# Optimization experiments

Hardware: AMD Instinct MI355X
Metric: run time of the kernel (lower is better)

Reference implementation:

```python
import jax, jax.numpy as jnp
import numpy as np

N_NODES = 100000


def setup_inputs() -> dict:
    key = jax.random.key(0)
    k1, k2, k3, k4, k5 = jax.random.split(key, 5)
    x = jax.random.normal(k1, (N_NODES, 256), dtype=jnp.float32)
    edge_index = jax.random.randint(k2, (2, 3200000), 0, N_NODES, dtype=jnp.int64)
    edge_weight = jax.random.uniform(k3, (3200000,), dtype=jnp.float32)
    W = jax.random.normal(k4, (256, 128), dtype=jnp.float32) / np.sqrt(256.0)
    b = jax.random.normal(k5, (128,), dtype=jnp.float32) * 0.01
    return {"x": x, "edge_index": edge_index, "edge_weight": edge_weight, "W": W, "b": b}


def reference(x, edge_index, edge_weight, W, b):
    # Dense linear projection: h = x @ W + b  -> [N, out_feats]
    h = x @ W + b
    # SpMM aggregation: out[dst] += w_e * h[src]
    src = edge_index[1]  # column indices (neighbors)
    dst = edge_index[0]  # row indices (output nodes)
    msgs = h[src] * edge_weight[:, None]  # [E, out_feats]
    out = jax.ops.segment_sum(msgs, dst, num_segments=x.shape[0])
    return out
```

## Files before the change

kernel.cpp:

```cpp
#include <hip/hip_runtime.h>

#define K_IN   256
#define N_OUT  128
#define BM     32
#define SCAN_CHUNK 1024
#define NBLK   512
#define BSHIFT 7
#define BNODES 128
#define CAP    8192
#define NKEY   2048
#define GEMM_BLOCKS 512

typedef short bf16x8 __attribute__((ext_vector_type(8)));
typedef float f32x4  __attribute__((ext_vector_type(4)));

static __device__ __forceinline__ unsigned short f2bf(float f) {
    unsigned u = __float_as_uint(f);
    unsigned r = (u + 0x7FFF + ((u >> 16) & 1)) >> 16;
    return (unsigned short)r;
}
static __device__ __forceinline__ float bf2f(unsigned short b) {
    return __uint_as_float(((unsigned)b) << 16);
}

__global__ __launch_bounds__(256) void hist_prep(
    const float* __restrict__ W, char* __restrict__ wbt,
    const int* __restrict__ ei, int* __restrict__ histG,
    int M, int E, int B, int chunk)
{
    __shared__ int bins[1024];
    const int tid = threadIdx.x;

    if (blockIdx.x >= NBLK) {
        const int t = (blockIdx.x - NBLK) * 256 + tid;
        if (t >= N_OUT * 32) return;
        const int n = t >> 5;
        const int c = t & 31;
        unsigned v[4];
#pragma unroll
        for (int p = 0; p < 4; ++p) {
            const unsigned lo = f2bf(W[(size_t)(c * 8 + 2 * p)     * N_OUT + n]);
            const unsigned hi = f2bf(W[(size_t)(c * 8 + 2 * p + 1) * N_OUT + n]);
            v[p] = lo | (hi << 16);
        }
        const int byte = n * 512 + ((c * 16) ^ ((n & 7) << 4));
        *reinterpret_cast<uint4*>(wbt + byte) = make_uint4(v[0], v[1], v[2], v[3]);
        return;
    }

    for (int i = tid; i < B; i += 256) bins[i] = 0;
    __syncthreads();
    const int beg = blockIdx.x * chunk;
    const int end = min(beg + chunk, E);
    for (int i = beg + tid; i < end; i += 256)
        atomicAdd(&bins[ei[i] >> BSHIFT], 1);
    __syncthreads();
    for (int i = tid; i < B; i += 256) histG[i * NBLK + blockIdx.x] = bins[i];
}

__global__ __launch_bounds__(256) void scan_block_sums(
    const int* __restrict__ cnt, int n, int* __restrict__ bsum)
{
    __shared__ int sd[256];
    const int base = blockIdx.x * SCAN_CHUNK + threadIdx.x * 4;
    int s = 0;
#pragma unroll
    for (int j = 0; j < 4; ++j) { const int idx = base + j; if (idx < n) s += cnt[idx]; }
    sd[threadIdx.x] = s; __syncthreads();
    for (int off = 128; off > 0; off >>= 1) {
        if (threadIdx.x < off) sd[threadIdx.x] += sd[threadIdx.x + off];
        __syncthreads();
    }
    if (threadIdx.x == 0) bsum[blockIdx.x] = sd[0];
}

__global__ __launch_bounds__(1024) void scan_sums(
    int* __restrict__ bsum, int nb, int* __restrict__ P, int n)
{
    __shared__ int sd[1024];
    const int t = threadIdx.x;
    const int v = (t < nb) ? bsum[t] : 0;
    sd[t] = v; __syncthreads();
    for (int off = 1; off < 1024; off <<= 1) {
        const int add = (t >= off) ? sd[t - off] : 0;
        __syncthreads();
        sd[t] += add;
        __syncthreads();
    }
    if (t < nb) bsum[t] = sd[t] - v;
    if (t == nb - 1) P[n] = sd[t];
}

__global__ __launch_bounds__(256) void scan_write_offsets(
    const int* __restrict__ cnt, int n, const int* __restrict__ bsum, int* __restrict__ P)
{
    __shared__ int sd[256];
    const int t = threadIdx.x;
    const int base = blockIdx.x * SCAN_CHUNK + t * 4;
    int v[4]; int s = 0;
#pragma unroll
    for (int j = 0; j < 4; ++j) { const int idx = base + j; v[j] = (idx < n) ? cnt[idx] : 0; s += v[j]; }
    sd[t] = s; __syncthreads();
    const int own = s;
    for (int off = 1; off < 256; off <<= 1) {
        const int add = (t >= off) ? sd[t - off] : 0;
        __syncthreads();
        sd[t] += add;
        __syncthreads();
    }
    int run = bsum[blockIdx.x] + (sd[t] - own);
#pragma unroll
    for (int j = 0; j < 4; ++j) {
        const int idx = base + j;
        if (idx < n) { P[idx] = run; run += v[j]; }
    }
}

__global__ __launch_bounds__(256) void gcn_gemm3(
    const float* __restrict__ x, const uint4* __restrict__ wbt,
    const float* __restrict__ bias, unsigned short* __restrict__ hb,
    int M, int ntiles)
{
    __shared__ uint4 smem4[81920 / 16];
    char* smem = (char*)smem4;
    const int tid = threadIdx.x;

    {
        uint4* wl = (uint4*)smem;
#pragma unroll
        for (int it = 0; it < 16; ++it) wl[it * 256 + tid] = wbt[it * 256 + tid];
    }

    const int lane = tid & 63;
    const int wv   = tid >> 6;
    const int wr   = wv >> 1;
    const int wc   = wv & 1;
    const int l15  = lane & 15;
    const int lk   = lane >> 4;

    const int  arow = wr * 16 + l15;
    const char* xrow = smem + 65536 + arow * 512;
    const int  aswz = (arow & 7) << 4;
    const int  bswz = (l15 & 7) << 4;
    const char* brow0 = smem + (size_t)(wc * 64 + l15) * 512;

    float bv[4];
#pragma unroll
    for (int j = 0; j < 4; ++j) bv[j] = bias[wc * 64 + j * 16 + l15];

    const int sr  = tid >> 3;
    const int sks = tid & 7;
    char* xbase   = smem + 65536 + sr * 512;
    const int swz = (sr & 7) << 4;

    for (int t = blockIdx.x; t < ntiles; t += gridDim.x) {
        const int row0 = t * BM;

        __syncthreads();
        {
            const int grow = row0 + sr;
            if (grow < M) {
                const float4* src = reinterpret_cast<const float4*>(x + (size_t)grow * K_IN + sks * 32);
#pragma unroll
                for (int q = 0; q < 8; ++q) {
                    const float4 f = src[q];
                    uint2 v;
                    v.x = (unsigned)f2bf(f.x) | ((unsigned)f2bf(f.y) << 16);
                    v.y = (unsigned)f2bf(f.z) | ((unsigned)f2bf(f.w) << 16);
                    const int kb = sks * 64 + q * 8;
                    *reinterpret_cast<uint2*>(xbase + (((kb & ~15) ^ swz) | (kb & 15))) = v;
                }
            } else {
                const uint2 z = make_uint2(0u, 0u);
#pragma unroll
                for (int q = 0; q < 8; ++q) {
                    const int kb = sks * 64 + q * 8;
                    *reinterpret_cast<uint2*>(xbase + (((kb & ~15) ^ swz) | (kb & 15))) = z;
                }
            }
        }
        __syncthreads();

        f32x4 acc[4] = {};
#pragma unroll
        for (int ks = 0; ks < 8; ++ks) {
            const int kb = ks * 64 + lk * 16;
            const bf16x8 a = *reinterpret_cast<const bf16x8*>(xrow + (kb ^ aswz));
            const int bk = kb ^ bswz;
#pragma unroll
            for (int j = 0; j < 4; ++j) {
                const bf16x8 b = *reinterpret_cast<const bf16x8*>(brow0 + j * (16 * 512) + bk);
                acc[j] = __builtin_amdgcn_mfma_f32_16x16x32_bf16(a, b, acc[j], 0, 0, 0);
            }
        }

#pragma unroll
        for (int j = 0; j < 4; ++j) {
            const int gcol = wc * 64 + j * 16 + l15;
#pragma unroll
            for (int r = 0; r < 4; ++r) {
                const int grow = row0 + wr * 16 + lk * 4 + r;
                if (grow < M)
                    hb[(size_t)grow * N_OUT + gcol] = f2bf(acc[j][r] + bv[j]);
            }
        }
    }
}

__global__ __launch_bounds__(256) void scatter_records(
    const int* __restrict__ ei, const float* __restrict__ ew, int E, int M, int B,
    const int* __restrict__ P, uint2* __restrict__ rec, int chunk)
{
    __shared__ int cur[1024];
    for (int i = threadIdx.x; i < B; i += 256) cur[i] = P[i * NBLK + blockIdx.x];
    __syncthreads();
    const int beg = blockIdx.x * chunk;
    const int end = min(beg + chunk, E);
    for (int i = beg + threadIdx.x; i < end; i += 256) {
        const int d = ei[i];
        const int s = ei[(size_t)E + i];
        const int pos = atomicAdd(&cur[d >> BSHIFT], 1);
        rec[pos] = make_uint2((unsigned)s | ((unsigned)(d & (BNODES - 1)) << 24),
                              __float_as_uint(ew[i]));
    }
}

__global__ __launch_bounds__(256) void sort_bucket(
    const int* __restrict__ P, uint2* __restrict__ rec,
    int* __restrict__ offsN, int* __restrict__ bflag, int M, int B)
{
    __shared__ uint2 srt[CAP];
    __shared__ int hist[NKEY];
    __shared__ int sd[256];

    const int b   = blockIdx.x;
    const int tid = threadIdx.x;
    const int beg = P[b * NBLK];
    const int end = P[(b + 1) * NBLK];
    const int cnt = end - beg;
    const int node0 = b << BSHIFT;

    for (int i = tid; i < NKEY; i += 256) hist[i] = 0;
    if (tid == 0) bflag[b] = (cnt <= CAP) ? 0 : 1;
    if (tid == 0 && b == B - 1) offsN[M] = end;
    __syncthreads();

    if (cnt > CAP) {
        if (tid < BNODES) {
            const int node = node0 + tid;
            if (node < M) offsN[node] = beg;
        }
        return;
    }

    for (int i = beg + tid; i < end; i += 256) {
        const uint2 r = rec[i];
        srt[i - beg] = r;
        const int key = ((r.x >> 24) << 4) | ((r.x & 0xFFFFFF) >> 13);
        atomicAdd(&hist[key], 1);
    }
    __syncthreads();

    const int base = tid * 8;
    int v[8]; int s = 0;
#pragma unroll
    for (int j = 0; j < 8; ++j) { v[j] = hist[base + j]; s += v[j]; }
    sd[tid] = s; __syncthreads();
    for (int off = 1; off < 256; off <<= 1) {
        const int add = (tid >= off) ? sd[tid - off] : 0;
        __syncthreads();
        sd[tid] += add;
        __syncthreads();
    }
    int run = sd[tid] - s;
#pragma unroll
    for (int j = 0; j < 8; ++j) { hist[base + j] = run; run += v[j]; }
    __syncthreads();

    if (tid < BNODES) {
        const int node = node0 + tid;
        if (node < M) offsN[node] = beg + hist[tid << 4];
    }
    __syncthreads();

    for (int i = tid; i < cnt; i += 256) {
        const uint2 r = srt[i];
        const int key = ((r.x >> 24) << 4) | ((r.x & 0xFFFFFF) >> 13);
        const int pos = atomicAdd(&hist[key], 1);
        rec[beg + pos] = r;
    }
}

__global__ __launch_bounds__(256) void gather_kernel(
    const int* __restrict__ offsN, const int* __restrict__ P,
    const int* __restrict__ bflag, const uint2* __restrict__ rec,
    const unsigned short* __restrict__ hb, float* __restrict__ out, int M)
{
    const int n = blockIdx.x * 4 + (threadIdx.x >> 6);
    if (n >= M) return;
    const int lane = threadIdx.x & 63;
    const int b = n >> BSHIFT;
    const unsigned* __restrict__ hb32 = reinterpret_cast<const unsigned*>(hb);

    float ax = 0.f, ay = 0.f;

    if (bflag[b] == 0) {
        const int beg = offsN[n], end = offsN[n + 1];
        int i = beg;
        for (; i + 16 <= end; i += 16) {
            unsigned u[16]; float w[16];
#pragma unroll
            for (int q = 0; q < 16; ++q) {
                const uint2 r = rec[i + q];
                w[q] = __uint_as_float(r.y);
                u[q] = hb32[(size_t)((r.x & 0xFFFFFF) << 6) + lane];
            }
#pragma unroll
            for (int q = 0; q < 16; ++q) {
                ax += w[q] * bf2f((unsigned short)u[q]);
                ay += w[q] * bf2f((unsigned short)(u[q] >> 16));
            }
        }
        for (; i + 8 <= end; i += 8) {
            unsigned u[8]; float w[8];
#pragma unroll
            for (int q = 0; q < 8; ++q) {
                const uint2 r = rec[i + q];
                w[q] = __uint_as_float(r.y);
                u[q] = hb32[(size_t)((r.x & 0xFFFFFF) << 6) + lane];
            }
#pragma unroll
            for (int q = 0; q < 8; ++q) {
                ax += w[q] * bf2f((unsigned short)u[q]);
                ay += w[q] * bf2f((unsigned short)(u[q] >> 16));
            }
        }
        for (; i < end; ++i) {
            const uint2 r = rec[i];
            const float w = __uint_as_float(r.y);
            const unsigned u = hb32[(size_t)((r.x & 0xFFFFFF) << 6) + lane];
            ax += w * bf2f((unsigned short)u);
            ay += w * bf2f((unsigned short)(u >> 16));
        }
    } else {
        const int beg = P[b * NBLK], end = P[(b + 1) * NBLK];
        const unsigned want = (unsigned)(n & (BNODES - 1));
        for (int i = beg; i < end; ++i) {
            const uint2 r = rec[i];
            if ((r.x >> 24) != want) continue;
            const float w = __uint_as_float(r.y);
            const unsigned u = hb32[(size_t)((r.x & 0xFFFFFF) << 6) + lane];
            ax += w * bf2f((unsigned short)u);
            ay += w * bf2f((unsigned short)(u >> 16));
        }
    }

    reinterpret_cast<float2*>(out + (size_t)n * N_OUT)[lane] = make_float2(ax, ay);
}

extern "C" void kernel_launch(void* const* d_in, const int* in_sizes, int n_in,
                              void* d_out, int out_size, void* d_ws, size_t ws_size,
                              hipStream_t stream)
{
    const float* x    = (const float*)d_in[0];
    const int*   ei   = (const int*)d_in[1];
    const float* ew   = (const float*)d_in[2];
    const float* W    = (const float*)d_in[3];
    const float* bias = (const float*)d_in[4];
    float* out = (float*)d_out;

    const int M = in_sizes[0] / K_IN;
    const int E = in_sizes[1] / 2;
    const int B = (M + BNODES - 1) >> BSHIFT;
    const int n = B * NBLK;
    const int nb = (n + SCAN_CHUNK - 1) / SCAN_CHUNK;
    const int chunk = (E + NBLK - 1) / NBLK;
    const int ntiles = (M + BM - 1) / BM;

    auto align256 = [](size_t v) { return (v + 255) & ~(size_t)255; };
    const size_t o_hb    = 0;
    const size_t o_hist  = align256(o_hb + (size_t)M * N_OUT * sizeof(unsigned short));
    const size_t o_P     = align256(o_hist + (size_t)n * sizeof(int));
    const size_t o_bsum  = align256(o_P + (size_t)(n + 1) * sizeof(int));
    const size_t o_offsN = align256(o_bsum + (size_t)1024 * sizeof(int));
    const size_t o_bflag = align256(o_offsN + (size_t)(M + 1) * sizeof(int));
    const size_t o_wbt   = align256(o_bflag + (size_t)B * sizeof(int));
    const size_t o_rec   = align256(o_wbt + (size_t)65536);

    unsigned short* hb    = (unsigned short*)((char*)d_ws + o_hb);
    int*            histG = (int*)((char*)d_ws + o_hist);
    int*            P     = (int*)((char*)d_ws + o_P);
    int*            bsum  = (int*)((char*)d_ws + o_bsum);
    int*            offsN = (int*)((char*)d_ws + o_offsN);
    int*            bflag = (int*)((char*)d_ws + o_bflag);
    char*           wbt   = (char*)d_ws + o_wbt;
    uint2*          rec   = (uint2*)((char*)d_ws + o_rec);

    hist_prep<<<NBLK + 16, 256, 0, stream>>>(W, wbt, ei, histG, M, E, B, chunk);
    gcn_gemm3<<<GEMM_BLOCKS, 256, 0, stream>>>(x, (const uint4*)wbt, bias, hb, M, ntiles);
    scan_block_sums<<<nb, 256, 0, stream>>>(histG, n, bsum);
    scan_sums<<<1, 1024, 0, stream>>>(bsum, nb, P, n);
    scan_write_offsets<<<nb, 256, 0, stream>>>(histG, n, bsum, P);
    scatter_records<<<NBLK, 256, 0, stream>>>(ei, ew, E, M, B, P, rec, chunk);
    sort_bucket<<<B, 256, 0, stream>>>(P, rec, offsN, bflag, M, B);
    gather_kernel<<<(M + 3) / 4, 256, 0, stream>>>(offsN, P, bflag, rec, hb, out, M);
}
```

Before: 240.6 us.

## Fuse GEMM and edge scatter into one kernel and swizzle gather blocks across XCDs

```diff
diff --git a/kernel.cpp b/kernel.cpp
--- a/kernel.cpp
+++ b/kernel.cpp
@@ -9,7 +9,7 @@
 #define BNODES 128
 #define CAP    8192
 #define NKEY   2048
-#define GEMM_BLOCKS 512
+#define NXCD   8
 
 typedef short bf16x8 __attribute__((ext_vector_type(8)));
 typedef float f32x4  __attribute__((ext_vector_type(4)));
@@ -116,14 +116,36 @@
     }
 }
 
-__global__ __launch_bounds__(256) void gcn_gemm3(
+__global__ __launch_bounds__(256) void gemm_scatter2(
     const float* __restrict__ x, const uint4* __restrict__ wbt,
     const float* __restrict__ bias, unsigned short* __restrict__ hb,
-    int M, int ntiles)
+    const int* __restrict__ ei, const float* __restrict__ ew,
+    const int* __restrict__ P, uint2* __restrict__ rec,
+    int M, int E, int B, int chunk, int ntiles)
 {
     __shared__ uint4 smem4[81920 / 16];
     char* smem = (char*)smem4;
     const int tid = threadIdx.x;
+
+    if (blockIdx.x & 1) {
+        int* cur = (int*)smem;
+        const int blk = blockIdx.x >> 1;
+        for (int i = tid; i < B; i += 256) cur[i] = P[i * NBLK + blk];
+        __syncthreads();
+        const int beg = blk * chunk;
+        const int end = min(beg + chunk, E);
+        for (int i = beg + tid; i < end; i += 256) {
+            const int d = ei[i];
+            const int s = ei[(size_t)E + i];
+            const int pos = atomicAdd(&cur[d >> BSHIFT], 1);
+            rec[pos] = make_uint2((unsigned)s | ((unsigned)(d & (BNODES - 1)) << 24),
+                                  __float_as_uint(ew[i]));
+        }
+        return;
+    }
+
+    const int gemm_id = blockIdx.x >> 1;
+    const int gstride = gridDim.x >> 1;
 
     {
         uint4* wl = (uint4*)smem;
@@ -153,7 +175,7 @@
     char* xbase   = smem + 65536 + sr * 512;
     const int swz = (sr & 7) << 4;
 
-    for (int t = blockIdx.x; t < ntiles; t += gridDim.x) {
+    for (int t = gemm_id; t < ntiles; t += gstride) {
         const int row0 = t * BM;
 
         __syncthreads();
@@ -207,24 +229,6 @@
     }
 }
 
-__global__ __launch_bounds__(256) void scatter_records(
-    const int* __restrict__ ei, const float* __restrict__ ew, int E, int M, int B,
-    const int* __restrict__ P, uint2* __restrict__ rec, int chunk)
-{
-    __shared__ int cur[1024];
-    for (int i = threadIdx.x; i < B; i += 256) cur[i] = P[i * NBLK + blockIdx.x];
-    __syncthreads();
-    const int beg = blockIdx.x * chunk;
-    const int end = min(beg + chunk, E);
-    for (int i = beg + threadIdx.x; i < end; i += 256) {
-        const int d = ei[i];
-        const int s = ei[(size_t)E + i];
-        const int pos = atomicAdd(&cur[d >> BSHIFT], 1);
-        rec[pos] = make_uint2((unsigned)s | ((unsigned)(d & (BNODES - 1)) << 24),
-                              __float_as_uint(ew[i]));
-    }
-}
-
 __global__ __launch_bounds__(256) void sort_bucket(
     const int* __restrict__ P, uint2* __restrict__ rec,
     int* __restrict__ offsN, int* __restrict__ bflag, int M, int B)
@@ -296,7 +300,14 @@
     const int* __restrict__ bflag, const uint2* __restrict__ rec,
     const unsigned short* __restrict__ hb, float* __restrict__ out, int M)
 {
-    const int n = blockIdx.x * 4 + (threadIdx.x >> 6);
+    const int nwg = gridDim.x;
+    const int q   = nwg / NXCD;
+    const int r   = nwg % NXCD;
+    const int xcd = blockIdx.x % NXCD;
+    const int idx = blockIdx.x / NXCD;
+    const int swz = (xcd < r ? xcd * (q + 1) : r * (q + 1) + (xcd - r) * q) + idx;
+
+    const int n = swz * 4 + (threadIdx.x >> 6);
     if (n >= M) return;
     const int lane = threadIdx.x & 63;
     const int b = n >> BSHIFT;
@@ -310,35 +321,35 @@
         for (; i + 16 <= end; i += 16) {
             unsigned u[16]; float w[16];
 #pragma unroll
-            for (int q = 0; q < 16; ++q) {
-                const uint2 r = rec[i + q];
-                w[q] = __uint_as_float(r.y);
-                u[q] = hb32[(size_t)((r.x & 0xFFFFFF) << 6) + lane];
-            }
-#pragma unroll
-            for (int q = 0; q < 16; ++q) {
-                ax += w[q] * bf2f((unsigned short)u[q]);
-                ay += w[q] * bf2f((unsigned short)(u[q] >> 16));
+            for (int qq = 0; qq < 16; ++qq) {
+                const uint2 rr = rec[i + qq];
+                w[qq] = __uint_as_float(rr.y);
+                u[qq] = hb32[(size_t)((rr.x & 0xFFFFFF) << 6) + lane];
+            }
+#pragma unroll
+            for (int qq = 0; qq < 16; ++qq) {
+                ax += w[qq] * bf2f((unsigned short)u[qq]);
+                ay += w[qq] * bf2f((unsigned short)(u[qq] >> 16));
             }
         }
         for (; i + 8 <= end; i += 8) {
             unsigned u[8]; float w[8];
 #pragma unroll
-            for (int q = 0; q < 8; ++q) {
-                const uint2 r = rec[i + q];
-                w[q] = __uint_as_float(r.y);
-                u[q] = hb32[(size_t)((r.x & 0xFFFFFF) << 6) + lane];
-            }
-#pragma unroll
-            for (int q = 0; q < 8; ++q) {
-                ax += w[q] * bf2f((unsigned short)u[q]);
-                ay += w[q] * bf2f((unsigned short)(u[q] >> 16));
+            for (int qq = 0; qq < 8; ++qq) {
+                const uint2 rr = rec[i + qq];
+                w[qq] = __uint_as_float(rr.y);
+                u[qq] = hb32[(size_t)((rr.x & 0xFFFFFF) << 6) + lane];
+            }
+#pragma unroll
+            for (int qq = 0; qq < 8; ++qq) {
+                ax += w[qq] * bf2f((unsigned short)u[qq]);
+                ay += w[qq] * bf2f((unsigned short)(u[qq] >> 16));
             }
         }
         for (; i < end; ++i) {
-            const uint2 r = rec[i];
-            const float w = __uint_as_float(r.y);
-            const unsigned u = hb32[(size_t)((r.x & 0xFFFFFF) << 6) + lane];
+            const uint2 rr = rec[i];
+            const float w = __uint_as_float(rr.y);
+            const unsigned u = hb32[(size_t)((rr.x & 0xFFFFFF) << 6) + lane];
             ax += w * bf2f((unsigned short)u);
             ay += w * bf2f((unsigned short)(u >> 16));
         }
@@ -346,10 +357,10 @@
         const int beg = P[b * NBLK], end = P[(b + 1) * NBLK];
         const unsigned want = (unsigned)(n & (BNODES - 1));
         for (int i = beg; i < end; ++i) {
-            const uint2 r = rec[i];
-            if ((r.x >> 24) != want) continue;
-            const float w = __uint_as_float(r.y);
-            const unsigned u = hb32[(size_t)((r.x & 0xFFFFFF) << 6) + lane];
+            const uint2 rr = rec[i];
+            if ((rr.x >> 24) != want) continue;
+            const float w = __uint_as_float(rr.y);
+            const unsigned u = hb32[(size_t)((rr.x & 0xFFFFFF) << 6) + lane];
             ax += w * bf2f((unsigned short)u);
             ay += w * bf2f((unsigned short)(u >> 16));
         }
@@ -397,11 +408,11 @@
     uint2*          rec   = (uint2*)((char*)d_ws + o_rec);
 
     hist_prep<<<NBLK + 16, 256, 0, stream>>>(W, wbt, ei, histG, M, E, B, chunk);
-    gcn_gemm3<<<GEMM_BLOCKS, 256, 0, stream>>>(x, (const uint4*)wbt, bias, hb, M, ntiles);
     scan_block_sums<<<nb, 256, 0, stream>>>(histG, n, bsum);
     scan_sums<<<1, 1024, 0, stream>>>(bsum, nb, P, n);
     scan_write_offsets<<<nb, 256, 0, stream>>>(histG, n, bsum, P);
-    scatter_records<<<NBLK, 256, 0, stream>>>(ei, ew, E, M, B, P, rec, chunk);
+    gemm_scatter2<<<2 * NBLK, 256, 0, stream>>>(
+        x, (const uint4*)wbt, bias, hb, ei, ew, P, rec, M, E, B, chunk, ntiles);
     sort_bucket<<<B, 256, 0, stream>>>(P, rec, offsN, bflag, M, B);
     gather_kernel<<<(M + 3) / 4, 256, 0, stream>>>(offsN, P, bflag, rec, hb, out, M);
 }
```

Measured after the change: 249.6 us. +3.7%, slower.
